# Kernel tuning notes

Hardware: AMD Instinct MI355X
Metric: run time of the kernel (lower is better)

The kernel has to match this reference:

```python
import jax, jax.numpy as jnp
import numpy as np

TEMP = 0.0005

def conv1d(x, w, b):
    # x: [B, Cin, T], w: [Cout, Cin, K] -> [B, Cout, T] with SAME padding
    out = jax.lax.conv_general_dilated(x, w, (1,), 'SAME', dimension_numbers=('NCH', 'OIH', 'NCH'))
    return out + b[None, :, None]

def setup_inputs() -> dict:
    key = jax.random.key(0)
    ks = jax.random.split(key, 24)
    B, Cs, T1 = 16, 80, 1000   # spec channels / mel frames
    Ct, T2 = 512, 200          # text channels / phonemes
    Ca, G = 80, 256            # attention channels / speaker embedding
    n = lambda i, shape: jax.random.normal(ks[i], shape, jnp.float32)
    w = lambda i, shape: n(i, shape) * 0.05
    return {
        'queries': n(0, (B, Cs, T1)),
        'keys': n(1, (B, Ct, T2)),
        'mask': jnp.ones((B, T2), jnp.int32),
        'attn_prior': jax.random.uniform(ks[2], (B, T1, T2), jnp.float32),
        'g': n(3, (B, G)),
        # key_proj: Conv(Ct -> 2Ct, k=3) -> ReLU -> Conv(2Ct -> Ca, k=1)
        'wk1': w(4, (2 * Ct, Ct, 3)), 'bk1': jnp.zeros((2 * Ct,), jnp.float32),
        'wk2': w(5, (Ca, 2 * Ct, 1)), 'bk2': jnp.zeros((Ca,), jnp.float32),
        # query_proj: Conv(Cs -> 2Cs, k=3) -> ReLU -> Conv(2Cs -> Cs, k=1) -> ReLU -> Conv(Cs -> Ca, k=1)
        'wq1': w(6, (2 * Cs, Cs, 3)), 'bq1': jnp.zeros((2 * Cs,), jnp.float32),
        'wq2': w(7, (Cs, 2 * Cs, 1)), 'bq2': jnp.zeros((Cs,), jnp.float32),
        'wq3': w(8, (Ca, Cs, 1)), 'bq3': jnp.zeros((Ca,), jnp.float32),
        # speaker projections (LinearNorm): gin -> n_text_channels / n_spec_channels
        'w_kspk': w(9, (Ct, G)), 'b_kspk': jnp.zeros((Ct,), jnp.float32),
        'w_qspk': w(10, (Cs, G)), 'b_qspk': jnp.zeros((Cs,), jnp.float32),
    }

def reference(queries, keys, mask, attn_prior, g, wk1, bk1, wk2, bk2, wq1, bq1, wq2, bq2, wq3, bq3, w_kspk, b_kspk, w_qspk, b_qspk):
    # speaker conditioning: same projected vector added at every time step
    keys = keys + (g @ w_kspk.T + b_kspk)[:, :, None]
    queries = queries + (g @ w_qspk.T + b_qspk)[:, :, None]
    # projections
    k_enc = conv1d(jax.nn.relu(conv1d(keys, wk1, bk1)), wk2, bk2)              # [B, Ca, T2]
    q = jax.nn.relu(conv1d(queries, wq1, bq1))
    q = jax.nn.relu(conv1d(q, wq2, bq2))
    q_enc = conv1d(q, wq3, bq3)                                                # [B, Ca, T1]
    # squared L2 distance via GEMM trick: |q|^2 + |k|^2 - 2 q.k  (same math as broadcast diff)
    q2 = jnp.sum(q_enc * q_enc, axis=1)[:, :, None]                            # [B, T1, 1]
    k2 = jnp.sum(k_enc * k_enc, axis=1)[:, None, :]                            # [B, 1, T2]
    qk = jnp.einsum('bct,bcs->bts', q_enc, k_enc)                              # [B, T1, T2]
    attn = (-TEMP * (q2 + k2 - 2.0 * qk))[:, None]                             # [B, 1, T1, T2]
    attn = jax.nn.log_softmax(attn, axis=3) + jnp.log(attn_prior[:, None] + 1e-8)
    attn_logprob = attn
    neg_inf = jnp.where(mask[:, None, None, :] == 0, -jnp.inf, 0.0)
    attn = jax.nn.softmax(attn + neg_inf, axis=3)
    return attn, attn_logprob
```

## Files before the change

### kernel.cpp

```cpp
#include <hip/hip_runtime.h>
#include <hip/hip_bf16.h>
#include <math.h>

#define NB 16
#define CS 80
#define T1 1000
#define CT 512
#define T2 200
#define CA 80
#define GD 256
#define C2T 1024
#define C2S 160
#define TEMP_F 0.0005f

typedef __attribute__((ext_vector_type(8))) short short8;
typedef __attribute__((ext_vector_type(4))) float floatx4;

__device__ __forceinline__ short f2bf(float x) {
    unsigned u = __builtin_bit_cast(unsigned, x);
    unsigned r = (u + 0x7fffu + ((u >> 16) & 1u)) >> 16;
    return (short)r;
}
__device__ __forceinline__ float bf2f(short s) {
    unsigned u = ((unsigned)(unsigned short)s) << 16;
    return __builtin_bit_cast(float, u);
}

__global__ __launch_bounds__(256) void spk_kernel(const float* __restrict__ g,
                           const float* __restrict__ w_kspk, const float* __restrict__ b_kspk,
                           const float* __restrict__ w_qspk, const float* __restrict__ b_qspk,
                           float* __restrict__ kspk, float* __restrict__ qspk) {
    int w = (blockIdx.x * 256 + threadIdx.x) >> 6;
    int lane = threadIdx.x & 63;
    const int NK = NB * CT;
    const float* wrow;
    float bias;
    float* dst;
    int b;
    if (w < NK) {
        b = w >> 9;
        int c = w & 511;
        wrow = w_kspk + (size_t)c * GD; bias = b_kspk[c]; dst = kspk + w;
    } else if (w < NK + NB * CS) {
        int i2 = w - NK;
        b = i2 / CS;
        int c = i2 - b * CS;
        wrow = w_qspk + (size_t)c * GD; bias = b_qspk[c]; dst = qspk + i2;
    } else return;
    float s = 0.f;
#pragma unroll
    for (int j = lane; j < GD; j += 64) s += g[b * GD + j] * wrow[j];
#pragma unroll
    for (int o = 1; o < 64; o <<= 1) s += __shfl_xor(s, o, 64);
    if (lane == 0) *dst = s + bias;
}

template <int C, int T>
__global__ __launch_bounds__(256) void addspkT_kernel(const float* __restrict__ in,
                                                      const float* __restrict__ spk,
                                                      short* __restrict__ outT) {
    __shared__ float S[32][65];
    const int t0 = blockIdx.x * 64, c0 = blockIdx.y * 32, b = blockIdx.z;
    const int tid = threadIdx.x;
    for (int i = tid; i < 32 * 64; i += 256) {
        int cl = i >> 6, tl = i & 63;
        int gc = c0 + cl, gt = t0 + tl;
        float v = 0.f;
        if (gc < C && gt < T) v = in[((size_t)b * C + gc) * T + gt] + spk[b * C + gc];
        S[cl][tl] = v;
    }
    __syncthreads();
    for (int i = tid; i < 64 * 32; i += 256) {
        int tl = i >> 5, cl = i & 31;
        int gt = t0 + tl, gc = c0 + cl;
        if (gc < C && gt < T) outT[((size_t)b * T + gt) * C + gc] = f2bf(S[cl][tl]);
    }
}

template <int COUT, int CIN, int KW, int COP, int CINP>
__global__ __launch_bounds__(256) void wpack_kernel(const float* __restrict__ w,
                                                    short* __restrict__ wp) {
    constexpr int NC32 = CINP / 32;
    constexpr int NFRAG = (COP / 16) * KW * NC32;
    int gid = blockIdx.x * 256 + threadIdx.x;
    int frag = gid >> 6, lane = gid & 63;
    if (frag >= NFRAG) return;
    int co16 = frag / (KW * NC32), rem = frag - co16 * (KW * NC32);
    int k = rem / NC32, ci32 = rem - k * NC32;
    int co = co16 * 16 + (lane & 15);
    int ci = ci32 * 32 + (lane >> 4) * 8;
    short8 v;
#pragma unroll
    for (int j = 0; j < 8; j++) {
        float f = 0.f;
        if (co < COUT && ci + j < CIN) f = w[((size_t)co * CIN + ci + j) * KW + k];
        v[j] = f2bf(f);
    }
    *(short8*)(wp + (size_t)frag * 512 + lane * 8) = v;
}

__global__ void convert3_kernel(const float* __restrict__ wk2, const float* __restrict__ wq2,
                                const float* __restrict__ wq3, short* __restrict__ wk2b,
                                short* __restrict__ wq2b, short* __restrict__ wq3b) {
    int i = blockIdx.x * 256 + threadIdx.x;
    const int N1 = CA * C2T, N2 = CA * C2S, N3 = CA * CS;
    if (i < N1) wk2b[i] = f2bf(wk2[i]);
    else if (i < N1 + N2) wq2b[i - N1] = f2bf(wq2[i - N1]);
    else if (i < N1 + N2 + N3) wq3b[i - N1 - N2] = f2bf(wq3[i - N1 - N2]);
}

template <int CIN, int COUT, int T, int KW, bool RELU, int CICH, int NC32T>
__global__ __launch_bounds__(256, 2) void conv_wg(const short* __restrict__ xT,
                                                  const short* __restrict__ wp,
                                                  const float* __restrict__ bias,
                                                  short* __restrict__ outT) {
    constexpr int TT = 128, COT = 64;
    constexpr int PAD = KW / 2;
    constexpr int XROWS = TT + KW - 1;
    constexpr int PITCH = CICH + 8;
    constexpr int NPC = CICH / 8;
    constexpr int NC32 = CICH / 32;
    constexpr int CINP = NC32T * 32;
    constexpr int NCHK = CINP / CICH;
    constexpr int NPIECE = XROWS * NPC;
    constexpr int NLD = (NPIECE + 255) / 256;
    constexpr int NBUF = (NCHK > 1) ? 2 : 1;
    __shared__ short Xs[NBUF * XROWS * PITCH];

    const int t0 = blockIdx.x * TT, co0 = blockIdx.y * COT, b = blockIdx.z;
    const int tid = threadIdx.x, wave = tid >> 6, lane = tid & 63;
    const int quad = lane >> 4, l16 = lane & 15;
    const int wt = wave * 32;
    const int co16_0 = co0 >> 4;
    const short* xb = xT + (size_t)b * T * CIN;

    floatx4 acc[4][2];
#pragma unroll
    for (int mi = 0; mi < 4; mi++)
#pragma unroll
        for (int ni = 0; ni < 2; ni++) acc[mi][ni] = (floatx4){0.f, 0.f, 0.f, 0.f};

    for (int i = tid; i < NPIECE; i += 256) {
        int r = i / NPC, p = i - r * NPC;
        int t = t0 + r - PAD, ci = p * 8;
        uint4 v = {0u, 0u, 0u, 0u};
        if ((unsigned)t < (unsigned)T && ci + 8 <= CIN)
            v = *(const uint4*)(xb + (size_t)t * CIN + ci);
        *(uint4*)(Xs + r * PITCH + p * 8) = v;
    }
    __syncthreads();

    for (int kc = 0; kc < NCHK; kc++) {
        uint4 tmp[NLD];
        if (kc + 1 < NCHK) {
            int ci0n = (kc + 1) * CICH;
#pragma unroll
            for (int ld = 0; ld < NLD; ld++) {
                int i = tid + ld * 256;
                tmp[ld] = (uint4){0u, 0u, 0u, 0u};
                if (i < NPIECE) {
                    int r = i / NPC, p = i - r * NPC;
                    int t = t0 + r - PAD, ci = ci0n + p * 8;
                    if ((unsigned)t < (unsigned)T && ci + 8 <= CIN)
                        tmp[ld] = *(const uint4*)(xb + (size_t)t * CIN + ci);
                }
            }
        }
        const short* Xb = Xs + (NBUF > 1 ? (kc & 1) : 0) * XROWS * PITCH;
#pragma unroll
        for (int k = 0; k < KW; k++) {
#pragma unroll
            for (int kk = 0; kk < NC32; kk++) {
                int ci32 = kc * NC32 + kk;
                short8 a[4];
#pragma unroll
                for (int mi = 0; mi < 4; mi++)
                    a[mi] = *(const short8*)(wp +
                        ((size_t)((co16_0 + mi) * KW + k) * NC32T + ci32) * 512 + lane * 8);
#pragma unroll
                for (int ni = 0; ni < 2; ni++) {
                    short8 bb = *(const short8*)(Xb + (wt + ni * 16 + l16 + k) * PITCH +
                                                 kk * 32 + quad * 8);
#pragma unroll
                    for (int mi = 0; mi < 4; mi++)
                        acc[mi][ni] = __builtin_amdgcn_mfma_f32_16x16x32_bf16(a[mi], bb,
                                                                              acc[mi][ni], 0, 0, 0);
                }
            }
        }
        if (kc + 1 < NCHK) {
            short* Xn = Xs + ((kc + 1) & 1) * XROWS * PITCH;
#pragma unroll
            for (int ld = 0; ld < NLD; ld++) {
                int i = tid + ld * 256;
                if (i < NPIECE) {
                    int r = i / NPC, p = i - r * NPC;
                    *(uint4*)(Xn + r * PITCH + p * 8) = tmp[ld];
                }
            }
            __syncthreads();
        }
    }
#pragma unroll
    for (int mi = 0; mi < 4; mi++) {
        int cb = co0 + mi * 16 + quad * 4;
        if (cb < COUT) {
            float4 bv = *(const float4*)(bias + cb);
#pragma unroll
            for (int ni = 0; ni < 2; ni++) {
                int t = t0 + wt + ni * 16 + l16;
                if (t < T) {
                    float v0 = acc[mi][ni][0] + bv.x, v1 = acc[mi][ni][1] + bv.y;
                    float v2 = acc[mi][ni][2] + bv.z, v3 = acc[mi][ni][3] + bv.w;
                    if (RELU) {
                        v0 = fmaxf(v0, 0.f); v1 = fmaxf(v1, 0.f);
                        v2 = fmaxf(v2, 0.f); v3 = fmaxf(v3, 0.f);
                    }
                    ushort4 o;
                    o.x = (unsigned short)f2bf(v0); o.y = (unsigned short)f2bf(v1);
                    o.z = (unsigned short)f2bf(v2); o.w = (unsigned short)f2bf(v3);
                    *(ushort4*)(outT + ((size_t)b * T + t) * COUT + cb) = o;
                }
            }
        }
    }
}

template <int K, int COUT, int NTOT, int NTILE, int SPLITK, int CICH>
__global__ __launch_bounds__(256) void gemm_splitk(const short* __restrict__ xT,
                                                   const short* __restrict__ w,
                                                   float* __restrict__ part) {
    constexpr int PITCH = CICH + 8, NPC = CICH / 8;
    constexpr int KSP = K / SPLITK;
    constexpr int NKC = KSP / CICH;
    constexpr int MT = COUT / 16;
    __shared__ short Xs[NTILE * PITCH];
    __shared__ short Ws[COUT * PITCH];
    const int n0 = blockIdx.x * NTILE;
    const int s = blockIdx.y;
    const int tid = threadIdx.x, wave = tid >> 6, lane = tid & 63;
    const int quad = lane >> 4, l16 = lane & 15;
    floatx4 acc[MT];
#pragma unroll
    for (int mi = 0; mi < MT; mi++) acc[mi] = (floatx4){0.f, 0.f, 0.f, 0.f};

    for (int kc = 0; kc < NKC; kc++) {
        const int ci0 = s * KSP + kc * CICH;
        if (kc) __syncthreads();
        for (int i = tid; i < NTILE * NPC; i += 256) {
            int r = i / NPC, p = i - r * NPC;
            *(uint4*)(Xs + r * PITCH + p * 8) =
                *(const uint4*)(xT + (size_t)(n0 + r) * K + ci0 + p * 8);
        }
        for (int i = tid; i < COUT * NPC; i += 256) {
            int r = i / NPC, p = i - r * NPC;
            *(uint4*)(Ws + r * PITCH + p * 8) =
                *(const uint4*)(w + (size_t)r * K + ci0 + p * 8);
        }
        __syncthreads();
#pragma unroll
        for (int kk = 0; kk < CICH / 32; kk++) {
            short8 bb = *(const short8*)(Xs + (wave * 16 + l16) * PITCH + kk * 32 + quad * 8);
#pragma unroll
            for (int mi = 0; mi < MT; mi++) {
                short8 a = *(const short8*)(Ws + (mi * 16 + l16) * PITCH + kk * 32 + quad * 8);
                acc[mi] = __builtin_amdgcn_mfma_f32_16x16x32_bf16(a, bb, acc[mi], 0, 0, 0);
            }
        }
    }
    int n = n0 + wave * 16 + l16;
#pragma unroll
    for (int mi = 0; mi < MT; mi++) {
        int cb = mi * 16 + quad * 4;
        float4 o = {acc[mi][0], acc[mi][1], acc[mi][2], acc[mi][3]};
        *(float4*)(part + ((size_t)s * NTOT + n) * COUT + cb) = o;
    }
}

template <int COUT, int NTOT, int SPLITK>
__global__ void combine_kernel(const float* __restrict__ part, const float* __restrict__ bias,
                               short* __restrict__ outT) {
    int i = blockIdx.x * 256 + threadIdx.x;
    if (i >= NTOT * (COUT / 4)) return;
    int n = i / (COUT / 4), c4 = i - n * (COUT / 4);
    int co = c4 * 4;
    float4 s = {0.f, 0.f, 0.f, 0.f};
#pragma unroll
    for (int k = 0; k < SPLITK; k++) {
        float4 v = *(const float4*)(part + ((size_t)k * NTOT + n) * COUT + co);
        s.x += v.x; s.y += v.y; s.z += v.z; s.w += v.w;
    }
    float4 b = *(const float4*)(bias + co);
    ushort4 o;
    o.x = (unsigned short)f2bf(s.x + b.x); o.y = (unsigned short)f2bf(s.y + b.y);
    o.z = (unsigned short)f2bf(s.z + b.z); o.w = (unsigned short)f2bf(s.w + b.w);
    *(ushort4*)(outT + (size_t)n * COUT + co) = o;
}

__global__ __launch_bounds__(256) void qconv23_kernel(const short* __restrict__ h1,
                                                      const short* __restrict__ w2,
                                                      const float* __restrict__ b2,
                                                      const short* __restrict__ w3,
                                                      const float* __restrict__ b3,
                                                      short* __restrict__ outT) {
    constexpr int K1 = 160, P1 = 168, NPC1 = 20;
    constexpr int P3 = 104, NPC3 = 12;
    __shared__ short Xs[64 * P1];
    __shared__ short W2s[80 * P1];
    __shared__ short W3s[80 * P3];
    __shared__ short Hs[64 * P3];
    const int n0 = blockIdx.x * 64;
    const int tid = threadIdx.x, wave = tid >> 6, lane = tid & 63;
    const int quad = lane >> 4, l16 = lane & 15;

    for (int i = tid; i < 64 * NPC1; i += 256) {
        int r = i / NPC1, p = i - r * NPC1;
        *(uint4*)(Xs + r * P1 + p * 8) = *(const uint4*)(h1 + (size_t)(n0 + r) * K1 + p * 8);
    }
    for (int i = tid; i < 80 * NPC1; i += 256) {
        int r = i / NPC1, p = i - r * NPC1;
        *(uint4*)(W2s + r * P1 + p * 8) = *(const uint4*)(w2 + (size_t)r * K1 + p * 8);
    }
    for (int i = tid; i < 80 * NPC3; i += 256) {
        int r = i / NPC3, p = i - r * NPC3;
        uint4 v = {0u, 0u, 0u, 0u};
        if (p < 10) v = *(const uint4*)(w3 + (size_t)r * 80 + p * 8);
        *(uint4*)(W3s + r * P3 + p * 8) = v;
    }
    if (tid < 128) *(uint4*)(Hs + (tid >> 1) * P3 + 80 + (tid & 1) * 8) = (uint4){0u, 0u, 0u, 0u};
    __syncthreads();

    floatx4 acc[5];
#pragma unroll
    for (int mi = 0; mi < 5; mi++) acc[mi] = (floatx4){0.f, 0.f, 0.f, 0.f};
#pragma unroll
    for (int kk = 0; kk < 5; kk++) {
        short8 bb = *(const short8*)(Xs + (wave * 16 + l16) * P1 + kk * 32 + quad * 8);
#pragma unroll
        for (int mi = 0; mi < 5; mi++) {
            short8 a = *(const short8*)(W2s + (mi * 16 + l16) * P1 + kk * 32 + quad * 8);
            acc[mi] = __builtin_amdgcn_mfma_f32_16x16x32_bf16(a, bb, acc[mi], 0, 0, 0);
        }
    }
#pragma unroll
    for (int mi = 0; mi < 5; mi++) {
        int cb = mi * 16 + quad * 4;
        float4 bv = *(const float4*)(b2 + cb);
        ushort4 o;
        o.x = (unsigned short)f2bf(fmaxf(acc[mi][0] + bv.x, 0.f));
        o.y = (unsigned short)f2bf(fmaxf(acc[mi][1] + bv.y, 0.f));
        o.z = (unsigned short)f2bf(fmaxf(acc[mi][2] + bv.z, 0.f));
        o.w = (unsigned short)f2bf(fmaxf(acc[mi][3] + bv.w, 0.f));
        *(ushort4*)(Hs + (wave * 16 + l16) * P3 + cb) = o;
    }
    __syncthreads();

    floatx4 acc3[5];
#pragma unroll
    for (int mi = 0; mi < 5; mi++) acc3[mi] = (floatx4){0.f, 0.f, 0.f, 0.f};
#pragma unroll
    for (int kk = 0; kk < 3; kk++) {
        short8 bb = *(const short8*)(Hs + (wave * 16 + l16) * P3 + kk * 32 + quad * 8);
#pragma unroll
        for (int mi = 0; mi < 5; mi++) {
            short8 a = *(const short8*)(W3s + (mi * 16 + l16) * P3 + kk * 32 + quad * 8);
            acc3[mi] = __builtin_amdgcn_mfma_f32_16x16x32_bf16(a, bb, acc3[mi], 0, 0, 0);
        }
    }
    int n = n0 + wave * 16 + l16;
#pragma unroll
    for (int mi = 0; mi < 5; mi++) {
        int cb = mi * 16 + quad * 4;
        float4 bv = *(const float4*)(b3 + cb);
        ushort4 o;
        o.x = (unsigned short)f2bf(acc3[mi][0] + bv.x);
        o.y = (unsigned short)f2bf(acc3[mi][1] + bv.y);
        o.z = (unsigned short)f2bf(acc3[mi][2] + bv.z);
        o.w = (unsigned short)f2bf(acc3[mi][3] + bv.w);
        *(ushort4*)(outT + (size_t)n * 80 + cb) = o;
    }
}

__device__ __forceinline__ float rmax16(float v) {
#pragma unroll
    for (int o = 1; o < 16; o <<= 1) v = fmaxf(v, __shfl_xor(v, o, 64));
    return v;
}
__device__ __forceinline__ float rsum16(float v) {
#pragma unroll
    for (int o = 1; o < 16; o <<= 1) v += __shfl_xor(v, o, 64);
    return v;
}

__global__ __launch_bounds__(256) void attn_kernel(const short* __restrict__ q_encT,
                                                   const short* __restrict__ k_encT,
                                                   const float* __restrict__ prior,
                                                   const int* __restrict__ mask,
                                                   float* __restrict__ out_attn,
                                                   float* __restrict__ out_logp) {
    constexpr int T2R = 208, PITCH = 104, NPC = 12;
    __shared__ short Kt[T2R * PITCH];
    __shared__ short Qs[64 * PITCH];
    __shared__ float k2s[T2R];
    __shared__ int msk[T2R];
    const int t10 = blockIdx.x * 64, b = blockIdx.y;
    const int tid = threadIdx.x;
    const int wave = tid >> 6, lane = tid & 63;
    const int quad = lane >> 4, l16 = lane & 15;

    for (int i = tid; i < T2R * NPC; i += 256) {
        int r = i / NPC, p = i - r * NPC;
        uint4 v = {0u, 0u, 0u, 0u};
        if (r < T2 && p < 10) v = *(const uint4*)(k_encT + ((size_t)b * T2 + r) * CA + p * 8);
        *(uint4*)(Kt + r * PITCH + p * 8) = v;
    }
    for (int i = tid; i < 64 * NPC; i += 256) {
        int r = i / NPC, p = i - r * NPC;
        int t1 = t10 + r;
        uint4 v = {0u, 0u, 0u, 0u};
        if (t1 < T1 && p < 10) v = *(const uint4*)(q_encT + ((size_t)b * T1 + t1) * CA + p * 8);
        *(uint4*)(Qs + r * PITCH + p * 8) = v;
    }
    if (tid < T2R) msk[tid] = (tid < T2) ? mask[b * T2 + tid] : 0;
    __syncthreads();
    for (int r = tid; r < T2R; r += 256) {
        float s = 0.f;
        for (int p = 0; p < NPC; p++) {
            short8 v = *(const short8*)(Kt + r * PITCH + p * 8);
#pragma unroll
            for (int j = 0; j < 8; j++) { float f = bf2f(v[j]); s += f * f; }
        }
        k2s[r] = s;
    }
    __syncthreads();

    floatx4 acc[13];
#pragma unroll
    for (int n = 0; n < 13; n++) acc[n] = (floatx4){0.f, 0.f, 0.f, 0.f};
#pragma unroll
    for (int kk = 0; kk < 3; kk++) {
        short8 a = *(const short8*)(Qs + (wave * 16 + l16) * PITCH + kk * 32 + quad * 8);
#pragma unroll
        for (int n = 0; n < 13; n++) {
            short8 bb = *(const short8*)(Kt + (n * 16 + l16) * PITCH + kk * 32 + quad * 8);
            acc[n] = __builtin_amdgcn_mfma_f32_16x16x32_bf16(a, bb, acc[n], 0, 0, 0);
        }
    }

#pragma unroll
    for (int r = 0; r < 4; r++) {
        int t1 = t10 + wave * 16 + quad * 4 + r;
        bool t1ok = t1 < T1;
        float s[13];
        float mx = -INFINITY;
#pragma unroll
        for (int n = 0; n < 13; n++) {
            int t2 = n * 16 + l16;
            float sv = -INFINITY;
            if (t2 < T2) sv = -TEMP_F * (k2s[t2] - 2.f * acc[n][r]);
            s[n] = sv;
            mx = fmaxf(mx, sv);
        }
        float m = rmax16(mx);
        float sume = 0.f;
#pragma unroll
        for (int n = 0; n < 13; n++) sume += (s[n] == -INFINITY) ? 0.f : __expf(s[n] - m);
        float logZ = __logf(rsum16(sume));
        float mx2 = -INFINITY;
#pragma unroll
        for (int n = 0; n < 13; n++) {
            int t2 = n * 16 + l16;
            float pr = 1.f;
            if (t1ok && t2 < T2) pr = prior[((size_t)b * T1 + t1) * T2 + t2];
            float lp = (t2 < T2) ? (s[n] - m - logZ + __logf(pr + 1e-8f)) : -INFINITY;
            s[n] = lp;
            float ms = (t2 < T2 && msk[t2] != 0) ? lp : -INFINITY;
            mx2 = fmaxf(mx2, ms);
        }
        float m2 = rmax16(mx2);
        float sume2 = 0.f;
        float e2v[13];
#pragma unroll
        for (int n = 0; n < 13; n++) {
            int t2 = n * 16 + l16;
            float ms = (t2 < T2 && msk[t2] != 0) ? s[n] : -INFINITY;
            float e = (ms == -INFINITY) ? 0.f : __expf(ms - m2);
            e2v[n] = e;
            sume2 += e;
        }
        float Z2 = rsum16(sume2);
        if (t1ok) {
#pragma unroll
            for (int n = 0; n < 13; n++) {
                int t2 = n * 16 + l16;
                if (t2 < T2) {
                    size_t o = ((size_t)b * T1 + t1) * T2 + t2;
                    out_attn[o] = e2v[n] / Z2;
                    out_logp[o] = s[n];
                }
            }
        }
    }
}

extern "C" void kernel_launch(void* const* d_in, const int* in_sizes, int n_in,
                              void* d_out, int out_size, void* d_ws, size_t ws_size,
                              hipStream_t stream) {
    const float* queries = (const float*)d_in[0];
    const float* keys    = (const float*)d_in[1];
    const int*   mask    = (const int*)d_in[2];
    const float* prior   = (const float*)d_in[3];
    const float* g       = (const float*)d_in[4];
    const float* wk1 = (const float*)d_in[5];
    const float* bk1 = (const float*)d_in[6];
    const float* wk2 = (const float*)d_in[7];
    const float* bk2 = (const float*)d_in[8];
    const float* wq1 = (const float*)d_in[9];
    const float* bq1 = (const float*)d_in[10];
    const float* wq2 = (const float*)d_in[11];
    const float* bq2 = (const float*)d_in[12];
    const float* wq3 = (const float*)d_in[13];
    const float* bq3 = (const float*)d_in[14];
    const float* w_kspk = (const float*)d_in[15];
    const float* b_kspk = (const float*)d_in[16];
    const float* w_qspk = (const float*)d_in[17];
    const float* b_qspk = (const float*)d_in[18];

    float* kspk = (float*)d_ws;
    float* qspk = kspk + 8192;
    short* wsS  = (short*)d_ws;
    short* xkT   = wsS + 20480;
    short* xqT   = wsS + 1658880;
    short* wk1p  = wsS + 2938880;
    short* wk2b  = wsS + 4511744;
    short* wq1p  = wsS + 4593664;
    short* wq2b  = wsS + 4648960;
    short* wq3b  = wsS + 4661760;
    short* k_encT = wsS + 4668160;
    short* q_encT = wsS + 4924160;
    float* part  = (float*)d_ws + 3102080;
    short* doS  = (short*)d_out;
    short* kh1T = doS;
    short* qh1T = doS + 3276800;

    spk_kernel<<<dim3((NB * (CT + CS) * 64 + 255) / 256), dim3(256), 0, stream>>>(
        g, w_kspk, b_kspk, w_qspk, b_qspk, kspk, qspk);
    wpack_kernel<C2T, CT, 3, C2T, CT>
        <<<dim3((64 * 3 * 16 * 64 + 255) / 256), dim3(256), 0, stream>>>(wk1, wk1p);
    wpack_kernel<C2S, CS, 3, 192, 96>
        <<<dim3((12 * 3 * 3 * 64 + 255) / 256), dim3(256), 0, stream>>>(wq1, wq1p);
    convert3_kernel<<<dim3((CA * (C2T + C2S + CS) + 255) / 256), dim3(256), 0, stream>>>(
        wk2, wq2, wq3, wk2b, wq2b, wq3b);
    addspkT_kernel<CT, T2><<<dim3(4, 16, NB), dim3(256), 0, stream>>>(keys, kspk, xkT);
    addspkT_kernel<CS, T1><<<dim3(16, 3, NB), dim3(256), 0, stream>>>(queries, qspk, xqT);

    conv_wg<CT, C2T, T2, 3, true, 64, 16>
        <<<dim3(2, 16, NB), dim3(256), 0, stream>>>(xkT, wk1p, bk1, kh1T);
    gemm_splitk<C2T, CA, NB * T2, 64, 8, 64>
        <<<dim3(50, 8), dim3(256), 0, stream>>>(kh1T, wk2b, part);
    combine_kernel<CA, NB * T2, 8>
        <<<dim3((NB * T2 * (CA / 4) + 255) / 256), dim3(256), 0, stream>>>(part, bk2, k_encT);
    conv_wg<CS, C2S, T1, 3, true, 96, 3>
        <<<dim3(8, 3, NB), dim3(256), 0, stream>>>(xqT, wq1p, bq1, qh1T);
    qconv23_kernel<<<dim3(NB * T1 / 64), dim3(256), 0, stream>>>(qh1T, wq2b, bq2, wq3b, bq3, q_encT);
    float* out_attn = (float*)d_out;
    float* out_logp = out_attn + (size_t)NB * T1 * T2;
    attn_kernel<<<dim3(16, NB), dim3(256), 0, stream>>>(q_encT, k_encT, prior, mask,
                                                        out_attn, out_logp);
}
```

Measured before the change: 220.1 us.

## Merge preprocessing, conv and GEMM launches into three fused grid-partitioned kernels

Cuts the launch count from about twelve kernels to four. Prep work (weight packing, speaker projection and transposes) now runs in one block-partitioned kernel, with the speaker projection computed inside each transpose block. The two k=3 convs share one launch, and the key 1x1 GEMM drops split-K and the combine pass in favour of a double-buffered full-K GEMM. That GEMM runs alongside the query conv2/3 in a single launch, with weights read in MFMA-packed fragments straight from global memory instead of staged through LDS. The aim is to remove launch gaps and tail serialization. The trade-offs are fewer blocks for the key GEMM and redundant speaker-projection dot products across blocks.

New measurement: 211.2 us. -4.1%, faster.

```diff
diff --git a/kernel.cpp b/kernel.cpp
--- a/kernel.cpp
+++ b/kernel.cpp
@@ -26,63 +26,12 @@
     return __builtin_bit_cast(float, u);
 }
 
-__global__ __launch_bounds__(256) void spk_kernel(const float* __restrict__ g,
-                           const float* __restrict__ w_kspk, const float* __restrict__ b_kspk,
-                           const float* __restrict__ w_qspk, const float* __restrict__ b_qspk,
-                           float* __restrict__ kspk, float* __restrict__ qspk) {
-    int w = (blockIdx.x * 256 + threadIdx.x) >> 6;
-    int lane = threadIdx.x & 63;
-    const int NK = NB * CT;
-    const float* wrow;
-    float bias;
-    float* dst;
-    int b;
-    if (w < NK) {
-        b = w >> 9;
-        int c = w & 511;
-        wrow = w_kspk + (size_t)c * GD; bias = b_kspk[c]; dst = kspk + w;
-    } else if (w < NK + NB * CS) {
-        int i2 = w - NK;
-        b = i2 / CS;
-        int c = i2 - b * CS;
-        wrow = w_qspk + (size_t)c * GD; bias = b_qspk[c]; dst = qspk + i2;
-    } else return;
-    float s = 0.f;
-#pragma unroll
-    for (int j = lane; j < GD; j += 64) s += g[b * GD + j] * wrow[j];
-#pragma unroll
-    for (int o = 1; o < 64; o <<= 1) s += __shfl_xor(s, o, 64);
-    if (lane == 0) *dst = s + bias;
-}
-
-template <int C, int T>
-__global__ __launch_bounds__(256) void addspkT_kernel(const float* __restrict__ in,
-                                                      const float* __restrict__ spk,
-                                                      short* __restrict__ outT) {
-    __shared__ float S[32][65];
-    const int t0 = blockIdx.x * 64, c0 = blockIdx.y * 32, b = blockIdx.z;
-    const int tid = threadIdx.x;
-    for (int i = tid; i < 32 * 64; i += 256) {
-        int cl = i >> 6, tl = i & 63;
-        int gc = c0 + cl, gt = t0 + tl;
-        float v = 0.f;
-        if (gc < C && gt < T) v = in[((size_t)b * C + gc) * T + gt] + spk[b * C + gc];
-        S[cl][tl] = v;
-    }
-    __syncthreads();
-    for (int i = tid; i < 64 * 32; i += 256) {
-        int tl = i >> 5, cl = i & 31;
-        int gt = t0 + tl, gc = c0 + cl;
-        if (gc < C && gt < T) outT[((size_t)b * T + gt) * C + gc] = f2bf(S[cl][tl]);
-    }
-}
-
 template <int COUT, int CIN, int KW, int COP, int CINP>
-__global__ __launch_bounds__(256) void wpack_kernel(const float* __restrict__ w,
-                                                    short* __restrict__ wp) {
+__device__ __forceinline__ void wpack_body(const float* __restrict__ w,
+                                           short* __restrict__ wp, int bid) {
     constexpr int NC32 = CINP / 32;
     constexpr int NFRAG = (COP / 16) * KW * NC32;
-    int gid = blockIdx.x * 256 + threadIdx.x;
+    int gid = bid * 256 + threadIdx.x;
     int frag = gid >> 6, lane = gid & 63;
     if (frag >= NFRAG) return;
     int co16 = frag / (KW * NC32), rem = frag - co16 * (KW * NC32);
@@ -99,21 +48,84 @@
     *(short8*)(wp + (size_t)frag * 512 + lane * 8) = v;
 }
 
-__global__ void convert3_kernel(const float* __restrict__ wk2, const float* __restrict__ wq2,
-                                const float* __restrict__ wq3, short* __restrict__ wk2b,
-                                short* __restrict__ wq2b, short* __restrict__ wq3b) {
-    int i = blockIdx.x * 256 + threadIdx.x;
-    const int N1 = CA * C2T, N2 = CA * C2S, N3 = CA * CS;
-    if (i < N1) wk2b[i] = f2bf(wk2[i]);
-    else if (i < N1 + N2) wq2b[i - N1] = f2bf(wq2[i - N1]);
-    else if (i < N1 + N2 + N3) wq3b[i - N1 - N2] = f2bf(wq3[i - N1 - N2]);
+template <int C, int T>
+__device__ __forceinline__ void addspkT_body(const float* __restrict__ in,
+                                             const float* __restrict__ g,
+                                             const float* __restrict__ w_spk,
+                                             const float* __restrict__ b_spk,
+                                             short* __restrict__ outT,
+                                             float* sm, int bx, int by, int b) {
+    float* spkS = sm;
+    float* S = sm + 32;
+    const int t0 = bx * 64, c0 = by * 32;
+    const int tid = threadIdx.x;
+    int cl = tid >> 3, part = tid & 7;
+    int c = c0 + cl;
+    float s = 0.f;
+    if (c < C) {
+        const float* wr = w_spk + (size_t)c * GD;
+        const float* gr = g + b * GD;
+        int j0 = part * 32;
+#pragma unroll
+        for (int j = 0; j < 32; j++) s += gr[j0 + j] * wr[j0 + j];
+    }
+    s += __shfl_xor(s, 1, 64); s += __shfl_xor(s, 2, 64); s += __shfl_xor(s, 4, 64);
+    if (part == 0) spkS[cl] = s + ((c < C) ? b_spk[c] : 0.f);
+    __syncthreads();
+    for (int i = tid; i < 32 * 64; i += 256) {
+        int cll = i >> 6, tl = i & 63;
+        int gc = c0 + cll, gt = t0 + tl;
+        float v = 0.f;
+        if (gc < C && gt < T) v = in[((size_t)b * C + gc) * T + gt] + spkS[cll];
+        S[cll * 65 + tl] = v;
+    }
+    __syncthreads();
+    for (int i = tid; i < 64 * 32; i += 256) {
+        int tl = i >> 5, cll = i & 31;
+        int gt = t0 + tl, gc = c0 + cll;
+        if (gc < C && gt < T) outT[((size_t)b * T + gt) * C + gc] = f2bf(S[cll * 65 + tl]);
+    }
+}
+
+__global__ __launch_bounds__(256) void prep_kernel(
+    const float* __restrict__ keys, const float* __restrict__ queries, const float* __restrict__ g,
+    const float* __restrict__ wk1, const float* __restrict__ wq1, const float* __restrict__ wk2,
+    const float* __restrict__ wq2, const float* __restrict__ wq3,
+    const float* __restrict__ w_kspk, const float* __restrict__ b_kspk,
+    const float* __restrict__ w_qspk, const float* __restrict__ b_qspk,
+    short* __restrict__ wk1p, short* __restrict__ wq1p, short* __restrict__ wk2p,
+    short* __restrict__ wq2p, short* __restrict__ wq3p,
+    short* __restrict__ xkT, short* __restrict__ xqT) {
+    __shared__ float sm[32 + 32 * 65];
+    int bid = blockIdx.x;
+    if (bid < 768) { wpack_body<C2T, CT, 3, C2T, CT>(wk1, wk1p, bid); return; }
+    bid -= 768;
+    if (bid < 27) { wpack_body<C2S, CS, 3, 192, 96>(wq1, wq1p, bid); return; }
+    bid -= 27;
+    if (bid < 40) { wpack_body<CA, C2T, 1, 80, 1024>(wk2, wk2p, bid); return; }
+    bid -= 40;
+    if (bid < 7) { wpack_body<CA, C2S, 1, 80, 160>(wq2, wq2p, bid); return; }
+    bid -= 7;
+    if (bid < 4) { wpack_body<CA, CS, 1, 80, 96>(wq3, wq3p, bid); return; }
+    bid -= 4;
+    if (bid < 1024) {
+        int bx = bid & 3, by = (bid >> 2) & 15, b = bid >> 6;
+        addspkT_body<CT, T2>(keys, g, w_kspk, b_kspk, xkT, sm, bx, by, b);
+        return;
+    }
+    bid -= 1024;
+    {
+        int bx = bid & 15, by = (bid >> 4) % 3, b = bid / 48;
+        addspkT_body<CS, T1>(queries, g, w_qspk, b_qspk, xqT, sm, bx, by, b);
+    }
 }
 
 template <int CIN, int COUT, int T, int KW, bool RELU, int CICH, int NC32T>
-__global__ __launch_bounds__(256, 2) void conv_wg(const short* __restrict__ xT,
-                                                  const short* __restrict__ wp,
-                                                  const float* __restrict__ bias,
-                                                  short* __restrict__ outT) {
+__device__ __forceinline__ void conv_body(const short* __restrict__ xT,
+                                          const short* __restrict__ wp,
+                                          const float* __restrict__ bias,
+                                          short* __restrict__ outT,
+                                          short* Xs, int bx, int by, int b) {
     constexpr int TT = 128, COT = 64;
     constexpr int PAD = KW / 2;
     constexpr int XROWS = TT + KW - 1;
@@ -124,10 +136,8 @@
     constexpr int NCHK = CINP / CICH;
     constexpr int NPIECE = XROWS * NPC;
     constexpr int NLD = (NPIECE + 255) / 256;
-    constexpr int NBUF = (NCHK > 1) ? 2 : 1;
-    __shared__ short Xs[NBUF * XROWS * PITCH];
-
-    const int t0 = blockIdx.x * TT, co0 = blockIdx.y * COT, b = blockIdx.z;
+
+    const int t0 = bx * TT, co0 = by * COT;
     const int tid = threadIdx.x, wave = tid >> 6, lane = tid & 63;
     const int quad = lane >> 4, l16 = lane & 15;
     const int wt = wave * 32;
@@ -152,7 +162,7 @@
 
     for (int kc = 0; kc < NCHK; kc++) {
         uint4 tmp[NLD];
-        if (kc + 1 < NCHK) {
+        if (NCHK > 1 && kc + 1 < NCHK) {
             int ci0n = (kc + 1) * CICH;
 #pragma unroll
             for (int ld = 0; ld < NLD; ld++) {
@@ -166,7 +176,7 @@
                 }
             }
         }
-        const short* Xb = Xs + (NBUF > 1 ? (kc & 1) : 0) * XROWS * PITCH;
+        const short* Xb = Xs + (NCHK > 1 ? (kc & 1) : 0) * XROWS * PITCH;
 #pragma unroll
         for (int k = 0; k < KW; k++) {
 #pragma unroll
@@ -188,7 +198,7 @@
                 }
             }
         }
-        if (kc + 1 < NCHK) {
+        if (NCHK > 1 && kc + 1 < NCHK) {
             short* Xn = Xs + ((kc + 1) & 1) * XROWS * PITCH;
 #pragma unroll
             for (int ld = 0; ld < NLD; ld++) {
@@ -226,90 +236,97 @@
     }
 }
 
-template <int K, int COUT, int NTOT, int NTILE, int SPLITK, int CICH>
-__global__ __launch_bounds__(256) void gemm_splitk(const short* __restrict__ xT,
-                                                   const short* __restrict__ w,
-                                                   float* __restrict__ part) {
-    constexpr int PITCH = CICH + 8, NPC = CICH / 8;
-    constexpr int KSP = K / SPLITK;
-    constexpr int NKC = KSP / CICH;
-    constexpr int MT = COUT / 16;
-    __shared__ short Xs[NTILE * PITCH];
-    __shared__ short Ws[COUT * PITCH];
-    const int n0 = blockIdx.x * NTILE;
-    const int s = blockIdx.y;
+__global__ __launch_bounds__(256, 2) void conv_kernel(
+    const short* __restrict__ xkT, const short* __restrict__ wk1p,
+    const float* __restrict__ bk1, short* __restrict__ kh1T,
+    const short* __restrict__ xqT, const short* __restrict__ wq1p,
+    const float* __restrict__ bq1, short* __restrict__ qh1T) {
+    __shared__ short sm[18720];
+    int bid = blockIdx.x;
+    if (bid < 512) {
+        int bx = bid & 1, by = (bid >> 1) & 15, b = bid >> 5;
+        conv_body<CT, C2T, T2, 3, true, 64, 16>(xkT, wk1p, bk1, kh1T, sm, bx, by, b);
+    } else {
+        int r = bid - 512;
+        int bx = r & 7, by = (r >> 3) % 3, b = r / 24;
+        conv_body<CS, C2S, T1, 3, true, 96, 3>(xqT, wq1p, bq1, qh1T, sm, bx, by, b);
+    }
+}
+
+__device__ __forceinline__ void kgemm_body(const short* __restrict__ xT,
+                                           const short* __restrict__ wp,
+                                           const float* __restrict__ bias,
+                                           short* __restrict__ outT, short* sm, int bid) {
+    constexpr int K = 1024, KCH = 128, PITCH = 136, NPC = 16, NCHK = 8;
+    const int n0 = bid * 64;
     const int tid = threadIdx.x, wave = tid >> 6, lane = tid & 63;
     const int quad = lane >> 4, l16 = lane & 15;
-    floatx4 acc[MT];
-#pragma unroll
-    for (int mi = 0; mi < MT; mi++) acc[mi] = (floatx4){0.f, 0.f, 0.f, 0.f};
-
-    for (int kc = 0; kc < NKC; kc++) {
-        const int ci0 = s * KSP + kc * CICH;
-        if (kc) __syncthreads();
-        for (int i = tid; i < NTILE * NPC; i += 256) {
-            int r = i / NPC, p = i - r * NPC;
-            *(uint4*)(Xs + r * PITCH + p * 8) =
-                *(const uint4*)(xT + (size_t)(n0 + r) * K + ci0 + p * 8);
-        }
-        for (int i = tid; i < COUT * NPC; i += 256) {
-            int r = i / NPC, p = i - r * NPC;
-            *(uint4*)(Ws + r * PITCH + p * 8) =
-                *(const uint4*)(w + (size_t)r * K + ci0 + p * 8);
-        }
-        __syncthreads();
-#pragma unroll
-        for (int kk = 0; kk < CICH / 32; kk++) {
-            short8 bb = *(const short8*)(Xs + (wave * 16 + l16) * PITCH + kk * 32 + quad * 8);
-#pragma unroll
-            for (int mi = 0; mi < MT; mi++) {
-                short8 a = *(const short8*)(Ws + (mi * 16 + l16) * PITCH + kk * 32 + quad * 8);
+    floatx4 acc[5];
+#pragma unroll
+    for (int mi = 0; mi < 5; mi++) acc[mi] = (floatx4){0.f, 0.f, 0.f, 0.f};
+
+    for (int i = tid; i < 64 * NPC; i += 256) {
+        int r = i / NPC, p = i - r * NPC;
+        *(uint4*)(sm + r * PITCH + p * 8) = *(const uint4*)(xT + (size_t)(n0 + r) * K + p * 8);
+    }
+    __syncthreads();
+    for (int kc = 0; kc < NCHK; kc++) {
+        uint4 tmp[4];
+        if (kc + 1 < NCHK) {
+            int ci0 = (kc + 1) * KCH;
+#pragma unroll
+            for (int ld = 0; ld < 4; ld++) {
+                int i = tid + ld * 256;
+                int r = i / NPC, p = i - r * NPC;
+                tmp[ld] = *(const uint4*)(xT + (size_t)(n0 + r) * K + ci0 + p * 8);
+            }
+        }
+        const short* Xb = sm + (kc & 1) * 64 * PITCH;
+#pragma unroll
+        for (int kk = 0; kk < 4; kk++) {
+            int ci32 = kc * 4 + kk;
+            short8 bb = *(const short8*)(Xb + (wave * 16 + l16) * PITCH + kk * 32 + quad * 8);
+#pragma unroll
+            for (int mi = 0; mi < 5; mi++) {
+                short8 a = *(const short8*)(wp + ((size_t)(mi * 32 + ci32)) * 512 + lane * 8);
                 acc[mi] = __builtin_amdgcn_mfma_f32_16x16x32_bf16(a, bb, acc[mi], 0, 0, 0);
             }
         }
+        if (kc + 1 < NCHK) {
+            short* Xn = sm + ((kc + 1) & 1) * 64 * PITCH;
+#pragma unroll
+            for (int ld = 0; ld < 4; ld++) {
+                int i = tid + ld * 256;
+                int r = i / NPC, p = i - r * NPC;
+                *(uint4*)(Xn + r * PITCH + p * 8) = tmp[ld];
+            }
+            __syncthreads();
+        }
     }
     int n = n0 + wave * 16 + l16;
 #pragma unroll
-    for (int mi = 0; mi < MT; mi++) {
+    for (int mi = 0; mi < 5; mi++) {
         int cb = mi * 16 + quad * 4;
-        float4 o = {acc[mi][0], acc[mi][1], acc[mi][2], acc[mi][3]};
-        *(float4*)(part + ((size_t)s * NTOT + n) * COUT + cb) = o;
-    }
-}
-
-template <int COUT, int NTOT, int SPLITK>
-__global__ void combine_kernel(const float* __restrict__ part, const float* __restrict__ bias,
-                               short* __restrict__ outT) {
-    int i = blockIdx.x * 256 + threadIdx.x;
-    if (i >= NTOT * (COUT / 4)) return;
-    int n = i / (COUT / 4), c4 = i - n * (COUT / 4);
-    int co = c4 * 4;
-    float4 s = {0.f, 0.f, 0.f, 0.f};
-#pragma unroll
-    for (int k = 0; k < SPLITK; k++) {
-        float4 v = *(const float4*)(part + ((size_t)k * NTOT + n) * COUT + co);
-        s.x += v.x; s.y += v.y; s.z += v.z; s.w += v.w;
-    }
-    float4 b = *(const float4*)(bias + co);
-    ushort4 o;
-    o.x = (unsigned short)f2bf(s.x + b.x); o.y = (unsigned short)f2bf(s.y + b.y);
-    o.z = (unsigned short)f2bf(s.z + b.z); o.w = (unsigned short)f2bf(s.w + b.w);
-    *(ushort4*)(outT + (size_t)n * COUT + co) = o;
-}
-
-__global__ __launch_bounds__(256) void qconv23_kernel(const short* __restrict__ h1,
-                                                      const short* __restrict__ w2,
-                                                      const float* __restrict__ b2,
-                                                      const short* __restrict__ w3,
-                                                      const float* __restrict__ b3,
-                                                      short* __restrict__ outT) {
-    constexpr int K1 = 160, P1 = 168, NPC1 = 20;
-    constexpr int P3 = 104, NPC3 = 12;
-    __shared__ short Xs[64 * P1];
-    __shared__ short W2s[80 * P1];
-    __shared__ short W3s[80 * P3];
-    __shared__ short Hs[64 * P3];
-    const int n0 = blockIdx.x * 64;
+        float4 bv = *(const float4*)(bias + cb);
+        ushort4 o;
+        o.x = (unsigned short)f2bf(acc[mi][0] + bv.x);
+        o.y = (unsigned short)f2bf(acc[mi][1] + bv.y);
+        o.z = (unsigned short)f2bf(acc[mi][2] + bv.z);
+        o.w = (unsigned short)f2bf(acc[mi][3] + bv.w);
+        *(ushort4*)(outT + (size_t)n * CA + cb) = o;
+    }
+}
+
+__device__ __forceinline__ void qconv23_body(const short* __restrict__ h1,
+                                             const short* __restrict__ w2p,
+                                             const float* __restrict__ b2,
+                                             const short* __restrict__ w3p,
+                                             const float* __restrict__ b3,
+                                             short* __restrict__ outT, short* sm, int bid) {
+    constexpr int K1 = 160, P1 = 168, NPC1 = 20, P3 = 104;
+    short* Xs = sm;
+    short* Hs = sm + 64 * P1;
+    const int n0 = bid * 64;
     const int tid = threadIdx.x, wave = tid >> 6, lane = tid & 63;
     const int quad = lane >> 4, l16 = lane & 15;
 
@@ -317,16 +334,6 @@
         int r = i / NPC1, p = i - r * NPC1;
         *(uint4*)(Xs + r * P1 + p * 8) = *(const uint4*)(h1 + (size_t)(n0 + r) * K1 + p * 8);
     }
-    for (int i = tid; i < 80 * NPC1; i += 256) {
-        int r = i / NPC1, p = i - r * NPC1;
-        *(uint4*)(W2s + r * P1 + p * 8) = *(const uint4*)(w2 + (size_t)r * K1 + p * 8);
-    }
-    for (int i = tid; i < 80 * NPC3; i += 256) {
-        int r = i / NPC3, p = i - r * NPC3;
-        uint4 v = {0u, 0u, 0u, 0u};
-        if (p < 10) v = *(const uint4*)(w3 + (size_t)r * 80 + p * 8);
-        *(uint4*)(W3s + r * P3 + p * 8) = v;
-    }
     if (tid < 128) *(uint4*)(Hs + (tid >> 1) * P3 + 80 + (tid & 1) * 8) = (uint4){0u, 0u, 0u, 0u};
     __syncthreads();
 
@@ -338,7 +345,7 @@
         short8 bb = *(const short8*)(Xs + (wave * 16 + l16) * P1 + kk * 32 + quad * 8);
 #pragma unroll
         for (int mi = 0; mi < 5; mi++) {
-            short8 a = *(const short8*)(W2s + (mi * 16 + l16) * P1 + kk * 32 + quad * 8);
+            short8 a = *(const short8*)(w2p + ((size_t)(mi * 5 + kk)) * 512 + lane * 8);
             acc[mi] = __builtin_amdgcn_mfma_f32_16x16x32_bf16(a, bb, acc[mi], 0, 0, 0);
         }
     }
@@ -363,7 +370,7 @@
         short8 bb = *(const short8*)(Hs + (wave * 16 + l16) * P3 + kk * 32 + quad * 8);
 #pragma unroll
         for (int mi = 0; mi < 5; mi++) {
-            short8 a = *(const short8*)(W3s + (mi * 16 + l16) * P3 + kk * 32 + quad * 8);
+            short8 a = *(const short8*)(w3p + ((size_t)(mi * 3 + kk)) * 512 + lane * 8);
             acc3[mi] = __builtin_amdgcn_mfma_f32_16x16x32_bf16(a, bb, acc3[mi], 0, 0, 0);
         }
     }
@@ -377,8 +384,20 @@
         o.y = (unsigned short)f2bf(acc3[mi][1] + bv.y);
         o.z = (unsigned short)f2bf(acc3[mi][2] + bv.z);
         o.w = (unsigned short)f2bf(acc3[mi][3] + bv.w);
-        *(ushort4*)(outT + (size_t)n * 80 + cb) = o;
-    }
+        *(ushort4*)(outT + (size_t)n * CA + cb) = o;
+    }
+}
+
+__global__ __launch_bounds__(256, 2) void gemm_kernel(
+    const short* __restrict__ kh1T, const short* __restrict__ wk2p,
+    const float* __restrict__ bk2, short* __restrict__ k_encT,
+    const short* __restrict__ qh1T, const short* __restrict__ wq2p,
+    const float* __restrict__ bq2, const short* __restrict__ wq3p,
+    const float* __restrict__ bq3, short* __restrict__ q_encT) {
+    __shared__ short sm[17408];
+    int bid = blockIdx.x;
+    if (bid < 50) kgemm_body(kh1T, wk2p, bk2, k_encT, sm, bid);
+    else qconv23_body(qh1T, wq2p, bq2, wq3p, bq3, q_encT, sm, bid - 50);
 }
 
 __device__ __forceinline__ float rmax16(float v) {
@@ -526,43 +545,28 @@
     const float* w_qspk = (const float*)d_in[17];
     const float* b_qspk = (const float*)d_in[18];
 
-    float* kspk = (float*)d_ws;
-    float* qspk = kspk + 8192;
-    short* wsS  = (short*)d_ws;
-    short* xkT   = wsS + 20480;
-    short* xqT   = wsS + 1658880;
-    short* wk1p  = wsS + 2938880;
-    short* wk2b  = wsS + 4511744;
-    short* wq1p  = wsS + 4593664;
-    short* wq2b  = wsS + 4648960;
-    short* wq3b  = wsS + 4661760;
-    short* k_encT = wsS + 4668160;
-    short* q_encT = wsS + 4924160;
-    float* part  = (float*)d_ws + 3102080;
+    short* wsS   = (short*)d_ws;
+    short* xkT   = wsS;
+    short* xqT   = wsS + 1638400;
+    short* wk1p  = wsS + 2918400;
+    short* wq1p  = wsS + 4491264;
+    short* wk2p  = wsS + 4546560;
+    short* wq2p  = wsS + 4628480;
+    short* wq3p  = wsS + 4641280;
+    short* k_encT = wsS + 4648960;
+    short* q_encT = wsS + 4904960;
     short* doS  = (short*)d_out;
     short* kh1T = doS;
     short* qh1T = doS + 3276800;
 
-    spk_kernel<<<dim3((NB * (CT + CS) * 64 + 255) / 256), dim3(256), 0, stream>>>(
-        g, w_kspk, b_kspk, w_qspk, b_qspk, kspk, qspk);
-    wpack_kernel<C2T, CT, 3, C2T, CT>
-        <<<dim3((64 * 3 * 16 * 64 + 255) / 256), dim3(256), 0, stream>>>(wk1, wk1p);
-    wpack_kernel<C2S, CS, 3, 192, 96>
-        <<<dim3((12 * 3 * 3 * 64 + 255) / 256), dim3(256), 0, stream>>>(wq1, wq1p);
-    convert3_kernel<<<dim3((CA * (C2T + C2S + CS) + 255) / 256), dim3(256), 0, stream>>>(
-        wk2, wq2, wq3, wk2b, wq2b, wq3b);
-    addspkT_kernel<CT, T2><<<dim3(4, 16, NB), dim3(256), 0, stream>>>(keys, kspk, xkT);
-    addspkT_kernel<CS, T1><<<dim3(16, 3, NB), dim3(256), 0, stream>>>(queries, qspk, xqT);
-
-    conv_wg<CT, C2T, T2, 3, true, 64, 16>
-        <<<dim3(2, 16, NB), dim3(256), 0, stream>>>(xkT, wk1p, bk1, kh1T);
-    gemm_splitk<C2T, CA, NB * T2, 64, 8, 64>
-        <<<dim3(50, 8), dim3(256), 0, stream>>>(kh1T, wk2b, part);
-    combine_kernel<CA, NB * T2, 8>
-        <<<dim3((NB * T2 * (CA / 4) + 255) / 256), dim3(256), 0, stream>>>(part, bk2, k_encT);
-    conv_wg<CS, C2S, T1, 3, true, 96, 3>
-        <<<dim3(8, 3, NB), dim3(256), 0, stream>>>(xqT, wq1p, bq1, qh1T);
-    qconv23_kernel<<<dim3(NB * T1 / 64), dim3(256), 0, stream>>>(qh1T, wq2b, bq2, wq3b, bq3, q_encT);
+    prep_kernel<<<dim3(2638), dim3(256), 0, stream>>>(
+        keys, queries, g, wk1, wq1, wk2, wq2, wq3,
+        w_kspk, b_kspk, w_qspk, b_qspk,
+        wk1p, wq1p, wk2p, wq2p, wq3p, xkT, xqT);
+    conv_kernel<<<dim3(896), dim3(256), 0, stream>>>(xkT, wk1p, bk1, kh1T,
+                                                     xqT, wq1p, bq1, qh1T);
+    gemm_kernel<<<dim3(300), dim3(256), 0, stream>>>(kh1T, wk2p, bk2, k_encT,
+                                                     qh1T, wq2p, bq2, wq3p, bq3, q_encT);
     float* out_attn = (float*)d_out;
     float* out_logp = out_attn + (size_t)NB * T1 * T2;
     attn_kernel<<<dim3(16, NB), dim3(256), 0, stream>>>(q_encT, k_encT, prior, mask,
```
